# Kernel optimization log

Measured on AMD Instinct MI355X. Metric: run time of the kernel, lower is better.

Reference implementation:

```python
import jax, jax.numpy as jnp
import numpy as np

N_NODES = 100000
N_EDGES = 500000
D = 128        # node feat dim == output dim
DT = 128       # time encoding dim
DE = 128       # edge feat dim
B = 300
K = 2
NN = 20
N_HEADS = 2
N_LAYERS = 2


def setup_inputs() -> dict:
    key = jax.random.key(0)
    ks = jax.random.split(key, 20)
    s = 0.05
    inp = {
        "node_features": jax.random.normal(ks[0], (N_NODES, D), jnp.float32) * s,
        "edge_features": jax.random.normal(ks[1], (N_EDGES, DE), jnp.float32) * s,
        "time_w": jax.random.normal(ks[2], (1, DT), jnp.float32),
        "time_b": jax.random.normal(ks[3], (DT,), jnp.float32),
        "Wq": jax.random.normal(ks[4], (N_LAYERS, D + DT, D), jnp.float32) * s,
        "Wk": jax.random.normal(ks[5], (N_LAYERS, D + DT + DE, D), jnp.float32) * s,
        "Wv": jax.random.normal(ks[6], (N_LAYERS, D + DT + DE, D), jnp.float32) * s,
        "Wo": jax.random.normal(ks[7], (N_LAYERS, D, D), jnp.float32) * s,
        "fc1": jax.random.normal(ks[8], (N_LAYERS, 2 * D, D), jnp.float32) * s,
        "fc2": jax.random.normal(ks[9], (N_LAYERS, D, D), jnp.float32) * s,
        "source_nodes": jax.random.randint(ks[10], (B,), 0, N_NODES),
        "timestamps": jax.random.uniform(ks[11], (B,), jnp.float32, 500.0, 1000.0),
        "neigh2": jax.random.randint(ks[12], (B, K, NN), 0, N_NODES),
        "eidx2": jax.random.randint(ks[13], (B, K, NN), 0, N_EDGES),
        "etimes2": jax.random.uniform(ks[14], (B, K, NN), jnp.float32, 0.0, 500.0),
        "neigh1": jax.random.randint(ks[15], (B * K * NN, K, NN), 0, N_NODES),
        "eidx1": jax.random.randint(ks[16], (B * K * NN, K, NN), 0, N_EDGES),
        "etimes1": jax.random.uniform(ks[17], (B * K * NN, K, NN), jnp.float32, 0.0, 500.0),
    }
    return inp


def reference(node_features, edge_features, time_w, time_b,
              Wq, Wk, Wv, Wo, fc1, fc2,
              source_nodes, timestamps,
              neigh2, eidx2, etimes2,
              neigh1, eidx1, etimes1):
    d = node_features.shape[1]
    dh = d // N_HEADS

    def time_enc(t):  # t: [...] -> [..., DT], TGAT-style cosine time encoding
        return jnp.cos(t[..., None] * time_w[0] + time_b)

    def hop_agg(layer, src_nodes, ts, neigh, eidx, etimes, neigh_emb):
        # neigh/eidx/etimes: [b, K, NN]; neigh_emb: [b, K, NN, d]
        b = src_nodes.shape[0]
        kn = K * NN
        src = node_features[src_nodes]                         # [b, d]
        src_t = time_enc(jnp.zeros((b,), ts.dtype))            # [b, DT]
        deltas = ts[:, None, None] - etimes                    # [b, K, NN]
        et = time_enc(deltas.reshape(b, kn))                   # [b, kn, DT]
        ef = edge_features[eidx].reshape(b, kn, -1)            # [b, kn, DE]
        ne = neigh_emb.reshape(b, kn, -1)                      # [b, kn, d]
        mask = neigh.reshape(b, kn) == 0                       # padded neighbors

        q = jnp.concatenate([src, src_t], axis=-1) @ Wq[layer]            # [b, d]
        kv_in = jnp.concatenate([ne, et, ef], axis=-1)                    # [b, kn, d+DT+DE]
        kk = kv_in @ Wk[layer]                                            # [b, kn, d]
        vv = kv_in @ Wv[layer]

        qh = q.reshape(b, N_HEADS, dh)
        kh = kk.reshape(b, kn, N_HEADS, dh)
        vh = vv.reshape(b, kn, N_HEADS, dh)
        scores = jnp.einsum('bhd,bnhd->bhn', qh, kh) / jnp.sqrt(jnp.float32(dh))
        scores = jnp.where(mask[:, None, :], jnp.float32(-1e9), scores)
        attn = jax.nn.softmax(scores, axis=-1)                            # [b, h, kn]
        out = jnp.einsum('bhn,bnhd->bhd', attn, vh).reshape(b, d) @ Wo[layer]
        merged = jnp.concatenate([out, src], axis=-1)                     # [b, 2d]
        return jax.nn.relu(merged @ fc1[layer]) @ fc2[layer]              # [b, d]

    # --- recursion unrolled (n_layers = 2) ---
    # level 0: raw node features of 2-hop neighbors
    b1 = neigh2.shape[0] * K * NN
    emb0 = node_features[neigh1.reshape(-1)].reshape(b1, K, NN, d)
    ts1 = jnp.repeat(timestamps, K * NN)
    # level 1 aggregation (attention_models[0])
    emb1 = hop_agg(0, neigh2.reshape(-1), ts1, neigh1, eidx1, etimes1, emb0)
    # level 2 aggregation (attention_models[1])
    emb2 = hop_agg(1, source_nodes, timestamps,
                   neigh2, eidx2, etimes2,
                   emb1.reshape(source_nodes.shape[0], K, NN, d))
    return emb2
```

## Files before the change

### kernel.cpp

```cpp
#include <hip/hip_runtime.h>
#include <cstdint>

typedef _Float16 half_t;
typedef _Float16 half8  __attribute__((ext_vector_type(8)));
typedef _Float16 half4_t __attribute__((ext_vector_type(4)));
typedef _Float16 h2f    __attribute__((ext_vector_type(2)));
typedef float    floatx4 __attribute__((ext_vector_type(4)));

#define KNN 40
#define KVPAD 124

#define WS_NF16    0ull
#define WS_EMB16   25600000ull
#define WS_WKVT    28672000ull
#define WS_WQ4     29065216ull
#define WS_W1A4    29196288ull
#define WS_W1B4    29327360ull
#define WS_W24     29458432ull
#define WS_QBIAS   29589504ull
#define WS_WOFTMP  29590528ull
#define WS_ZERO    29721600ull
#define WS_EF16    29721856ull
#define WS_TOTAL_FULL (WS_EF16 + 128000000ull)

__device__ __forceinline__ void ld16(const void* g, void* l) {
  __builtin_amdgcn_global_load_lds(
      (const __attribute__((address_space(1))) unsigned int*)(uintptr_t)g,
      (__attribute__((address_space(3))) unsigned int*)(uintptr_t)l, 16, 0, 0);
}

__device__ __forceinline__ float dot4(half4_t a, half4_t b, float s) {
  s = __builtin_amdgcn_fdot2((h2f){a[0], a[1]}, (h2f){b[0], b[1]}, s, false);
  s = __builtin_amdgcn_fdot2((h2f){a[2], a[3]}, (h2f){b[2], b[3]}, s, false);
  return s;
}

__global__ __launch_bounds__(256) void cvt_kernel(
    const float* __restrict__ src, half_t* __restrict__ dst, int n8) {
  int stride = gridDim.x * 256;
  for (int i = blockIdx.x * 256 + threadIdx.x; i < n8; i += stride) {
    float4 a = *((const float4*)src + 2 * (size_t)i);
    float4 b = *((const float4*)src + 2 * (size_t)i + 1);
    half8 h;
    h[0] = (half_t)a.x; h[1] = (half_t)a.y; h[2] = (half_t)a.z; h[3] = (half_t)a.w;
    h[4] = (half_t)b.x; h[5] = (half_t)b.y; h[6] = (half_t)b.z; h[7] = (half_t)b.w;
    *((half8*)dst + i) = h;
  }
}

#define PK_DECODE(t) int l = (t) >> 14; int u = (t) & 16383; \
  int d4 = u >> 9; int v = u & 511; int j = v >> 2; int e = v & 3;

__global__ __launch_bounds__(256) void precompute_w(
    const float* __restrict__ Wq, const float* __restrict__ Wk,
    const float* __restrict__ Wv, const float* __restrict__ Wo,
    const float* __restrict__ fc1, const float* __restrict__ fc2,
    const float* __restrict__ time_b,
    half_t* __restrict__ WkvT, float* __restrict__ qbias,
    float* __restrict__ woftmp, half_t* __restrict__ Wq4,
    half_t* __restrict__ W1b4, half_t* __restrict__ W24,
    half_t* __restrict__ zrow)
{
  int blk = blockIdx.x, tid = threadIdx.x;
  if (blk < 768) {
    int t = blk * 256 + tid;
    int l = t / 98304;
    int r = t - l * 98304;
    int n = r / 384;
    int k = r - n * 384;
    float vv = (n < 128) ? Wk[l * 49152 + k * 128 + n]
                         : Wv[l * 49152 + k * 128 + (n - 128)];
    WkvT[t] = (half_t)vv;
  } else if (blk == 768) {
    if (tid < 128) zrow[tid] = (half_t)0.f;
    int l = tid >> 7, j = tid & 127;
    float s = 0.f;
    for (int d = 0; d < 128; ++d)
      s += cosf(time_b[d]) * Wq[l * 32768 + (128 + d) * 128 + j];
    qbias[l * 128 + j] = s;
  } else if (blk < 897) {
    int t = (blk - 769) * 256 + tid;
    int l = t >> 14;
    int r = t & 16383;
    int dd = r >> 7, j = r & 127;
    float s = 0.f;
    for (int m = 0; m < 128; ++m)
      s += Wo[l * 16384 + dd * 128 + m] * fc1[l * 32768 + m * 128 + j];
    woftmp[t] = s;
  } else if (blk < 1025) {
    int t = (blk - 897) * 256 + tid;
    PK_DECODE(t);
    Wq4[t] = (half_t)Wq[l * 32768 + (4 * d4 + e) * 128 + j];
  } else if (blk < 1153) {
    int t = (blk - 1025) * 256 + tid;
    PK_DECODE(t);
    W1b4[t] = (half_t)fc1[l * 32768 + (128 + 4 * d4 + e) * 128 + j];
  } else {
    int t = (blk - 1153) * 256 + tid;
    PK_DECODE(t);
    W24[t] = (half_t)fc2[l * 16384 + (4 * d4 + e) * 128 + j];
  }
}

__global__ __launch_bounds__(256) void precompute_w2(
    const float* __restrict__ woftmp, half_t* __restrict__ W1a4) {
  int t = blockIdx.x * 256 + threadIdx.x;
  PK_DECODE(t);
  W1a4[t] = (half_t)woftmp[l * 16384 + (4 * d4 + e) * 128 + j];
}

template <bool EF16, bool L1DIR>
__global__ __launch_bounds__(512, 4) void hop_kernel(
    const float*  __restrict__ nf,
    const half_t* __restrict__ ne16,
    const half_t* __restrict__ ef16,
    const float*  __restrict__ ef32,
    const int*    __restrict__ src_idx,
    const float*  __restrict__ tsv,
    const int*    __restrict__ neigh,
    const int*    __restrict__ eidx,
    const float*  __restrict__ etimes,
    const float*  __restrict__ tw,
    const float*  __restrict__ tb,
    const half_t* __restrict__ Wq4_l,
    const float*  __restrict__ qbias_l,
    const half_t* __restrict__ WkvT_l,
    const half_t* __restrict__ W1a4_l,
    const half_t* __restrict__ W1b4_l,
    const half_t* __restrict__ W24_l,
    const half_t* __restrict__ zrow,
    half_t* __restrict__ out16,
    float*  __restrict__ out32)
{
  __shared__ __align__(16) char smem[71360];
  half_t* BTs  = (half_t*)(smem + 32768);
  half_t* kvT  = (half_t*)(smem + 32768);
  float*  tw_s = (float*)(smem + 65536);
  float*  tb_s = (float*)(smem + 66048);
  float*  qs   = (float*)(smem + 66560);
  half_t* s16  = (half_t*)(smem + 68096);
  half_t* aO16 = (half_t*)(smem + 68864);
  half_t* h116 = (half_t*)(smem + 69632);
  float*  scs  = (float*)(smem + 70400);

  const int tid = threadIdx.x;
  const int bbase = blockIdx.x * 3;
  const int lane = tid & 63, wv = tid >> 6;
  const int l15 = lane & 15, q4 = lane >> 4;
  const int wm = (wv & 1) * 64, wn = (wv >> 1) * 64;

  if (tid < 128) { tw_s[tid] = tw[tid]; tb_s[tid] = tb[tid]; }
  if (tid < 96) {
    int g = tid >> 5, d4 = tid & 31;
    float4 v4 = *(const float4*)(nf + (size_t)src_idx[bbase + g] * 128 + d4 * 4);
    half4_t h;
    h[0] = (half_t)v4.x; h[1] = (half_t)v4.y; h[2] = (half_t)v4.z; h[3] = (half_t)v4.w;
    *(half4_t*)(s16 + g * 128 + d4 * 4) = h;
  }

  int neighval = 1;
  if (tid < 240) {
    int g = tid / 80, rem = tid - g * 80, n = rem % 40;
    neighval = neigh[(bbase + g) * KNN + n];
  }

  const int r = wv * 16 + l15;
  const bool valid = (r < 120);
  float dval = 0.f;
  const half_t* pNE = zrow + q4 * 8;
  const half_t* pEF = zrow + q4 * 8;
  if (valid) {
    int g = r / 40, n = r - g * 40;
    int bg = bbase + g;
    int rowidx = bg * KNN + n;
    dval = tsv[L1DIR ? bg : (bg / 40)] - etimes[rowidx];
    pNE = (L1DIR ? ne16 + (size_t)rowidx * 128
                 : ne16 + (size_t)neigh[rowidx] * 128) + q4 * 8;
    if (EF16) pEF = ef16 + (size_t)eidx[rowidx] * 128 + q4 * 8;
  }
  const float* gbe32 = nullptr;
  const int rr = tid >> 2, pp = tid & 3;
  if (!EF16 && rr < 120) {
    int g2 = rr / 40, n2 = rr - g2 * 40;
    gbe32 = ef32 + (size_t)eidx[(bbase + g2) * KNN + n2] * 128 + pp * 8;
  }

  const half_t* bBase = WkvT_l + (size_t)(2 * wv * 16 + l15) * 384 + q4 * 8;

  floatx4 acc[4][4];
  #pragma unroll
  for (int mi = 0; mi < 4; ++mi)
    #pragma unroll
    for (int ni = 0; ni < 4; ++ni) acc[mi][ni] = (floatx4){0.f, 0.f, 0.f, 0.f};

  auto issB = [&](int s, char* bb) {
    int kc = (s < 4) ? s : (s < 8 ? s + 4 : s - 4);
    const half_t* bp = bBase + kc * 32;
    ld16(bp,        bb + wv * 2048);
    ld16(bp + 6144, bb + wv * 2048 + 1024);
  };
  auto issA = [&](int s, char* ab) {
    const half_t* p = (s < 4) ? pNE + s * 32 : pEF + (s - 4) * 32;
    ld16(p, ab + wv * 1024);
  };
  auto cosA = [&](int s, char* ab) {
    int cb = (s - 8) * 32 + q4 * 8;
    half8 h;
    #pragma unroll
    for (int j = 0; j < 8; ++j) {
      float ang = __builtin_fmaf(dval, tw_s[cb + j], tb_s[cb + j]);
      h[j] = valid ? (half_t)__cosf(ang) : (half_t)0.f;
    }
    *(half8*)(ab + wv * 1024 + lane * 16) = h;
  };
  auto efA32 = [&](int s, char* ab) {
    half8 h = {};
    if (rr < 120) {
      const float* gb = gbe32 + (s - 4) * 32;
      float4 v0 = ((const float4*)gb)[0];
      float4 v1 = ((const float4*)gb)[1];
      h[0] = (half_t)v0.x; h[1] = (half_t)v0.y; h[2] = (half_t)v0.z; h[3] = (half_t)v0.w;
      h[4] = (half_t)v1.x; h[5] = (half_t)v1.y; h[6] = (half_t)v1.z; h[7] = (half_t)v1.w;
    }
    *(half8*)(ab + (rr >> 4) * 1024 + pp * 256 + (rr & 15) * 16) = h;
  };
  auto mfma_step = [&](const char* ab, const char* bb) {
    const half_t* A  = (const half_t*)ab;
    const half_t* Bp = (const half_t*)bb;
    half8 a[4];
    #pragma unroll
    for (int mi = 0; mi < 4; ++mi)
      a[mi] = *(const half8*)(A + ((wv & 1) * 4 + mi) * 512 + q4 * 128 + l15 * 8);
    #pragma unroll
    for (int ni = 0; ni < 4; ++ni) {
      half8 bfr = *(const half8*)(Bp + (((wn >> 4) + ni) * 512) + q4 * 128 + l15 * 8);
      #pragma unroll
      for (int mi = 0; mi < 4; ++mi)
        acc[mi][ni] = __builtin_amdgcn_mfma_f32_16x16x32_f16(a[mi], bfr, acc[mi][ni], 0, 0, 0);
    }
  };
  auto stageW = [&](const half_t* wsrc, char* dst) {
    const char* sw = (const char*)wsrc + wv * 4096 + lane * 16;
    char* dw = dst + wv * 4096;
    ld16(sw, dw); ld16(sw + 1024, dw + 1024);
    ld16(sw + 2048, dw + 2048); ld16(sw + 3072, dw + 3072);
  };

#define AB(i) (smem + (i) * 8192)
#define BB(i) (smem + 32768 + (i) * 16384)
#define FENCE asm volatile("" ::: "memory")

  FENCE;
  issB(0, BB(0)); issB(1, BB(1));
  issA(0, AB(0)); issA(1, AB(1)); issA(2, AB(2)); issA(3, AB(3));
  asm volatile("s_waitcnt lgkmcnt(0)" ::: "memory");
  __builtin_amdgcn_s_barrier(); FENCE;

#define HSTEP(s, WE, WF, ...)                                                   \
  asm volatile("s_waitcnt vmcnt(%0) lgkmcnt(0)" :: "i"(EF16 ? (WE) : (WF))      \
               : "memory");                                                     \
  __builtin_amdgcn_s_barrier(); FENCE;                                          \
  mfma_step(AB((s) & 3), BB((s) & 1));                                          \
  FENCE; __builtin_amdgcn_s_barrier(); FENCE;                                   \
  __VA_ARGS__

  HSTEP(0, 3, 3, issB(2, BB(0)); if constexpr (EF16) issA(4, AB(0)); else efA32(4, AB(0));)
  HSTEP(1, 5, 4, issB(3, BB(1)); if constexpr (EF16) issA(5, AB(1)); else efA32(5, AB(1));)
  HSTEP(2, 7, 5, issB(4, BB(0)); if constexpr (EF16) issA(6, AB(2)); else efA32(6, AB(2));)
  HSTEP(3, 9, 6, issB(5, BB(1)); if constexpr (EF16) issA(7, AB(3)); else efA32(7, AB(3));)
  HSTEP(4, 4, 2, issB(6, BB(0)); cosA(8, AB(0));)
  HSTEP(5, 3, 2, issB(7, BB(1)); cosA(9, AB(1));)
  HSTEP(6, 2, 2, issB(8, BB(0)); cosA(10, AB(2));)
  HSTEP(7, 2, 2, issB(9, BB(1)); cosA(11, AB(3));)
  HSTEP(8, 2, 2, issB(10, BB(0));)
  HSTEP(9, 2, 2, issB(11, BB(1));)
  HSTEP(10, 2, 2, )
  HSTEP(11, 0, 0, )
#undef HSTEP

  stageW(W1a4_l, smem);

  if (wv < 4) {
    #pragma unroll
    for (int mi = 0; mi < 4; ++mi) {
      int row0 = wm + mi * 16 + q4 * 4;
      if (row0 < 120) {
        #pragma unroll
        for (int ni = 0; ni < 4; ++ni) {
          int col = wn + ni * 16 + l15;
          half4_t h;
          h[0] = (half_t)acc[mi][ni][0]; h[1] = (half_t)acc[mi][ni][1];
          h[2] = (half_t)acc[mi][ni][2]; h[3] = (half_t)acc[mi][ni][3];
          *(half4_t*)(kvT + col * KVPAD + row0) = h;
        }
      }
    }
  }

  if (tid < 384) {
    int gq = tid >> 7, jj = tid & 127;
    float s = qbias_l[jj];
    #pragma unroll 8
    for (int d4 = 0; d4 < 32; ++d4) {
      half4_t w = *(const half4_t*)(Wq4_l + (d4 * 128 + jj) * 4);
      half4_t a = *(const half4_t*)(s16 + gq * 128 + d4 * 4);
      s = dot4(w, a, s);
    }
    qs[gq * 128 + jj] = s;
  }
  asm volatile("s_waitcnt lgkmcnt(0)" ::: "memory");
  __builtin_amdgcn_s_barrier(); FENCE;

  if (tid < 240) {
    int g = tid / 80;
    int rem = tid - g * 80;
    int hh = rem / 40;
    int n = rem - hh * 40;
    const float* qrow = qs + g * 128 + hh * 64;
    int row = g * 40 + n;
    float s = 0.f;
    #pragma unroll 8
    for (int d = 0; d < 64; ++d)
      s += qrow[d] * (float)kvT[(hh * 64 + d) * KVPAD + row];
    scs[tid] = (neighval == 0) ? -1e9f : s * 0.125f;
  }
  asm volatile("s_waitcnt lgkmcnt(0)" ::: "memory");
  __builtin_amdgcn_s_barrier(); FENCE;

  if (wv < 6) {
    float v = (lane < 40) ? scs[wv * 40 + lane] : -1e30f;
    float m = v;
    #pragma unroll
    for (int o = 32; o; o >>= 1) m = fmaxf(m, __shfl_xor(m, o));
    float e = (lane < 40) ? __expf(v - m) : 0.f;
    float ssum = e;
    #pragma unroll
    for (int o = 32; o; o >>= 1) ssum += __shfl_xor(ssum, o);
    if (lane < 40) scs[wv * 40 + lane] = e / ssum;
  }
  if (wv >= 4) {
    #pragma unroll
    for (int mi = 0; mi < 4; ++mi) {
      int row0 = wm + mi * 16 + q4 * 4;
      if (row0 < 120) {
        #pragma unroll
        for (int ni = 0; ni < 4; ++ni) {
          int col = wn - 128 + ni * 16 + l15;
          half4_t h;
          h[0] = (half_t)acc[mi][ni][0]; h[1] = (half_t)acc[mi][ni][1];
          h[2] = (half_t)acc[mi][ni][2]; h[3] = (half_t)acc[mi][ni][3];
          *(half4_t*)(kvT + col * KVPAD + row0) = h;
        }
      }
    }
  }
  asm volatile("s_waitcnt lgkmcnt(0)" ::: "memory");
  __builtin_amdgcn_s_barrier(); FENCE;

  if (tid < 384) {
    int g = tid >> 7, dcol = tid & 127, hh = dcol >> 6;
    const float* attn = scs + (g * 2 + hh) * 40;
    const half_t* vcol = kvT + dcol * KVPAD + g * 40;
    float s = 0.f;
    #pragma unroll 8
    for (int n = 0; n < 40; ++n) s += attn[n] * (float)vcol[n];
    aO16[g * 128 + dcol] = (half_t)s;
  }
  asm volatile("s_waitcnt lgkmcnt(0)" ::: "memory");
  __builtin_amdgcn_s_barrier(); FENCE;

  stageW(W1b4_l, (char*)BTs);
  asm volatile("s_waitcnt vmcnt(4)" ::: "memory");
  __builtin_amdgcn_s_barrier(); FENCE;

  float p1 = 0.f;
  if (tid < 384) {
    int g = tid >> 7, jj = tid & 127;
    #pragma unroll 8
    for (int d4 = 0; d4 < 32; ++d4) {
      half4_t w = *(const half4_t*)((const half_t*)smem + (d4 * 128 + jj) * 4);
      half4_t a = *(const half4_t*)(aO16 + g * 128 + d4 * 4);
      p1 = dot4(w, a, p1);
    }
  }
  FENCE; __builtin_amdgcn_s_barrier(); FENCE;

  stageW(W24_l, smem);
  asm volatile("s_waitcnt vmcnt(4)" ::: "memory");
  __builtin_amdgcn_s_barrier(); FENCE;
  if (tid < 384) {
    int g = tid >> 7, jj = tid & 127;
    float p2 = p1;
    #pragma unroll 8
    for (int d4 = 0; d4 < 32; ++d4) {
      half4_t w = *(const half4_t*)(BTs + (d4 * 128 + jj) * 4);
      half4_t a = *(const half4_t*)(s16 + g * 128 + d4 * 4);
      p2 = dot4(w, a, p2);
    }
    h116[g * 128 + jj] = (half_t)fmaxf(p2, 0.f);
  }
  asm volatile("s_waitcnt vmcnt(0) lgkmcnt(0)" ::: "memory");
  __builtin_amdgcn_s_barrier(); FENCE;

  if (tid < 384) {
    int g = tid >> 7, ii = tid & 127;
    float s = 0.f;
    #pragma unroll 8
    for (int j4 = 0; j4 < 32; ++j4) {
      half4_t w = *(const half4_t*)((const half_t*)smem + (j4 * 128 + ii) * 4);
      half4_t a = *(const half4_t*)(h116 + g * 128 + j4 * 4);
      s = dot4(w, a, s);
    }
    if (L1DIR) out32[(size_t)(bbase + g) * 128 + ii] = s;
    else       out16[(size_t)(bbase + g) * 128 + ii] = (half_t)s;
  }
#undef AB
#undef BB
#undef FENCE
}

extern "C" void kernel_launch(void* const* d_in, const int* in_sizes, int n_in,
                              void* d_out, int out_size, void* d_ws, size_t ws_size,
                              hipStream_t stream) {
  const float* nf      = (const float*)d_in[0];
  const float* ef      = (const float*)d_in[1];
  const float* tw      = (const float*)d_in[2];
  const float* tb      = (const float*)d_in[3];
  const float* Wq      = (const float*)d_in[4];
  const float* Wk      = (const float*)d_in[5];
  const float* Wv      = (const float*)d_in[6];
  const float* Wo      = (const float*)d_in[7];
  const float* fc1     = (const float*)d_in[8];
  const float* fc2     = (const float*)d_in[9];
  const int*   srcn    = (const int*)d_in[10];
  const float* ts      = (const float*)d_in[11];
  const int*   neigh2  = (const int*)d_in[12];
  const int*   eidx2   = (const int*)d_in[13];
  const float* etimes2 = (const float*)d_in[14];
  const int*   neigh1  = (const int*)d_in[15];
  const int*   eidx1   = (const int*)d_in[16];
  const float* etimes1 = (const float*)d_in[17];

  char* ws = (char*)d_ws;
  half_t* nf16   = (half_t*)(ws + WS_NF16);
  half_t* emb116 = (half_t*)(ws + WS_EMB16);
  half_t* WkvT16 = (half_t*)(ws + WS_WKVT);
  half_t* Wq4    = (half_t*)(ws + WS_WQ4);
  half_t* W1a4   = (half_t*)(ws + WS_W1A4);
  half_t* W1b4   = (half_t*)(ws + WS_W1B4);
  half_t* W24    = (half_t*)(ws + WS_W24);
  float*  qbias  = (float*)(ws + WS_QBIAS);
  float*  woftmp = (float*)(ws + WS_WOFTMP);
  half_t* zrow   = (half_t*)(ws + WS_ZERO);
  half_t* ef16   = (half_t*)(ws + WS_EF16);

  bool full = (ws_size >= WS_TOTAL_FULL);

  cvt_kernel<<<dim3(2048), dim3(256), 0, stream>>>(nf, nf16, 1600000);
  if (full)
    cvt_kernel<<<dim3(4096), dim3(256), 0, stream>>>(ef, ef16, 8000000);
  precompute_w<<<dim3(1281), dim3(256), 0, stream>>>(
      Wq, Wk, Wv, Wo, fc1, fc2, tb, WkvT16, qbias, woftmp, Wq4, W1b4, W24, zrow);
  precompute_w2<<<dim3(128), dim3(256), 0, stream>>>(woftmp, W1a4);

  if (full) {
    hop_kernel<true, false><<<dim3(4000), dim3(512), 0, stream>>>(
        nf, nf16, ef16, ef, neigh2, ts, neigh1, eidx1, etimes1, tw, tb,
        Wq4, qbias, WkvT16, W1a4, W1b4, W24, zrow, emb116, nullptr);
    hop_kernel<true, true><<<dim3(100), dim3(512), 0, stream>>>(
        nf, emb116, ef16, ef, srcn, ts, neigh2, eidx2, etimes2, tw, tb,
        Wq4 + 16384, qbias + 128, WkvT16 + 98304, W1a4 + 16384, W1b4 + 16384,
        W24 + 16384, zrow, emb116, (float*)d_out);
  } else {
    hop_kernel<false, false><<<dim3(4000), dim3(512), 0, stream>>>(
        nf, nf16, ef16, ef, neigh2, ts, neigh1, eidx1, etimes1, tw, tb,
        Wq4, qbias, WkvT16, W1a4, W1b4, W24, zrow, emb116, nullptr);
    hop_kernel<false, true><<<dim3(100), dim3(512), 0, stream>>>(
        nf, emb116, ef16, ef, srcn, ts, neigh2, eidx2, etimes2, tw, tb,
        Wq4 + 16384, qbias + 128, WkvT16 + 98304, W1a4 + 16384, W1b4 + 16384,
        W24 + 16384, zrow, emb116, (float*)d_out);
  }
}
```

Before: 706.4 us.

## Use MFMA for output MLP and read weights directly from global memory

The post-attention fc1/fc2 matvecs, previously done as scalar fdot2 loops over LDS-staged weights, become 16x16x32 MFMA tiles. Only 3 of 16 rows are real, and B fragments are loaded straight from global memory. The LDS weight staging and its barriers are removed. Packed weight layouts widen from 4 to 8 halves so the Q projection can use half8 loads, and the score and AV loops are vectorised with float4 and half4 loads. This trades redundant MFMA rows and uncoalesced global weight reads for fewer barriers and fewer scalar dot instructions.

```diff
diff --git a/kernel.cpp b/kernel.cpp
--- a/kernel.cpp
+++ b/kernel.cpp
@@ -29,9 +29,11 @@
       (__attribute__((address_space(3))) unsigned int*)(uintptr_t)l, 16, 0, 0);
 }
 
-__device__ __forceinline__ float dot4(half4_t a, half4_t b, float s) {
+__device__ __forceinline__ float dot8(half8 a, half8 b, float s) {
   s = __builtin_amdgcn_fdot2((h2f){a[0], a[1]}, (h2f){b[0], b[1]}, s, false);
   s = __builtin_amdgcn_fdot2((h2f){a[2], a[3]}, (h2f){b[2], b[3]}, s, false);
+  s = __builtin_amdgcn_fdot2((h2f){a[4], a[5]}, (h2f){b[4], b[5]}, s, false);
+  s = __builtin_amdgcn_fdot2((h2f){a[6], a[7]}, (h2f){b[6], b[7]}, s, false);
   return s;
 }
 
@@ -48,8 +50,8 @@
   }
 }
 
-#define PK_DECODE(t) int l = (t) >> 14; int u = (t) & 16383; \
-  int d4 = u >> 9; int v = u & 511; int j = v >> 2; int e = v & 3;
+#define PK8_DECODE(t) int l = (t) >> 14; int u = (t) & 16383; \
+  int d8 = u >> 10; int v = u & 1023; int j = v >> 3; int e = v & 7;
 
 __global__ __launch_bounds__(256) void precompute_w(
     const float* __restrict__ Wq, const float* __restrict__ Wk,
@@ -89,24 +91,24 @@
     woftmp[t] = s;
   } else if (blk < 1025) {
     int t = (blk - 897) * 256 + tid;
-    PK_DECODE(t);
-    Wq4[t] = (half_t)Wq[l * 32768 + (4 * d4 + e) * 128 + j];
+    PK8_DECODE(t);
+    Wq4[t] = (half_t)Wq[l * 32768 + (8 * d8 + e) * 128 + j];
   } else if (blk < 1153) {
     int t = (blk - 1025) * 256 + tid;
-    PK_DECODE(t);
-    W1b4[t] = (half_t)fc1[l * 32768 + (128 + 4 * d4 + e) * 128 + j];
+    PK8_DECODE(t);
+    W1b4[t] = (half_t)fc1[l * 32768 + (128 + 8 * d8 + e) * 128 + j];
   } else {
     int t = (blk - 1153) * 256 + tid;
-    PK_DECODE(t);
-    W24[t] = (half_t)fc2[l * 16384 + (4 * d4 + e) * 128 + j];
+    PK8_DECODE(t);
+    W24[t] = (half_t)fc2[l * 16384 + (8 * d8 + e) * 128 + j];
   }
 }
 
 __global__ __launch_bounds__(256) void precompute_w2(
     const float* __restrict__ woftmp, half_t* __restrict__ W1a4) {
   int t = blockIdx.x * 256 + threadIdx.x;
-  PK_DECODE(t);
-  W1a4[t] = (half_t)woftmp[l * 16384 + (4 * d4 + e) * 128 + j];
+  PK8_DECODE(t);
+  W1a4[t] = (half_t)woftmp[l * 16384 + (8 * d8 + e) * 128 + j];
 }
 
 template <bool EF16, bool L1DIR>
@@ -239,12 +241,6 @@
         acc[mi][ni] = __builtin_amdgcn_mfma_f32_16x16x32_f16(a[mi], bfr, acc[mi][ni], 0, 0, 0);
     }
   };
-  auto stageW = [&](const half_t* wsrc, char* dst) {
-    const char* sw = (const char*)wsrc + wv * 4096 + lane * 16;
-    char* dw = dst + wv * 4096;
-    ld16(sw, dw); ld16(sw + 1024, dw + 1024);
-    ld16(sw + 2048, dw + 2048); ld16(sw + 3072, dw + 3072);
-  };
 
 #define AB(i) (smem + (i) * 8192)
 #define BB(i) (smem + 32768 + (i) * 16384)
@@ -278,7 +274,6 @@
   HSTEP(11, 0, 0, )
 #undef HSTEP
 
-  stageW(W1a4_l, smem);
 
   if (wv < 4) {
     #pragma unroll
@@ -300,11 +295,11 @@
   if (tid < 384) {
     int gq = tid >> 7, jj = tid & 127;
     float s = qbias_l[jj];
-    #pragma unroll 8
-    for (int d4 = 0; d4 < 32; ++d4) {
-      half4_t w = *(const half4_t*)(Wq4_l + (d4 * 128 + jj) * 4);
-      half4_t a = *(const half4_t*)(s16 + gq * 128 + d4 * 4);
-      s = dot4(w, a, s);
+    #pragma unroll
+    for (int d8 = 0; d8 < 16; ++d8) {
+      half8 w = *(const half8*)(Wq4_l + (d8 * 128 + jj) * 8);
+      half8 a = *(const half8*)(s16 + gq * 128 + d8 * 8);
+      s = dot8(w, a, s);
     }
     qs[gq * 128 + jj] = s;
   }
@@ -316,12 +311,18 @@
     int rem = tid - g * 80;
     int hh = rem / 40;
     int n = rem - hh * 40;
-    const float* qrow = qs + g * 128 + hh * 64;
+    const float4* qrow4 = (const float4*)(qs + g * 128 + hh * 64);
     int row = g * 40 + n;
     float s = 0.f;
-    #pragma unroll 8
-    for (int d = 0; d < 64; ++d)
-      s += qrow[d] * (float)kvT[(hh * 64 + d) * KVPAD + row];
+    #pragma unroll
+    for (int d4 = 0; d4 < 16; ++d4) {
+      float4 qv = qrow4[d4];
+      const half_t* kp = kvT + (hh * 64 + d4 * 4) * KVPAD + row;
+      s += qv.x * (float)kp[0];
+      s += qv.y * (float)kp[KVPAD];
+      s += qv.z * (float)kp[2 * KVPAD];
+      s += qv.w * (float)kp[3 * KVPAD];
+    }
     scs[tid] = (neighval == 0) ? -1e9f : s * 0.125f;
   }
   asm volatile("s_waitcnt lgkmcnt(0)" ::: "memory");
@@ -359,60 +360,81 @@
 
   if (tid < 384) {
     int g = tid >> 7, dcol = tid & 127, hh = dcol >> 6;
-    const float* attn = scs + (g * 2 + hh) * 40;
+    const float4* at4 = (const float4*)(scs + (g * 2 + hh) * 40);
     const half_t* vcol = kvT + dcol * KVPAD + g * 40;
     float s = 0.f;
-    #pragma unroll 8
-    for (int n = 0; n < 40; ++n) s += attn[n] * (float)vcol[n];
+    #pragma unroll
+    for (int n4 = 0; n4 < 10; ++n4) {
+      float4 a4 = at4[n4];
+      half4_t v = *(const half4_t*)(vcol + n4 * 4);
+      s += a4.x * (float)v[0] + a4.y * (float)v[1]
+         + a4.z * (float)v[2] + a4.w * (float)v[3];
+    }
     aO16[g * 128 + dcol] = (half_t)s;
   }
   asm volatile("s_waitcnt lgkmcnt(0)" ::: "memory");
   __builtin_amdgcn_s_barrier(); FENCE;
 
-  stageW(W1b4_l, (char*)BTs);
-  asm volatile("s_waitcnt vmcnt(4)" ::: "memory");
+  {
+    const int ar = (l15 < 3) ? l15 : 0;
+    if (wv < 4) {
+      const int ni0 = wv * 2;
+      floatx4 facc0 = (floatx4){0.f, 0.f, 0.f, 0.f};
+      floatx4 facc1 = (floatx4){0.f, 0.f, 0.f, 0.f};
+      #pragma unroll
+      for (int kc = 0; kc < 4; ++kc) {
+        half8 a1 = *(const half8*)(aO16 + ar * 128 + kc * 32 + q4 * 8);
+        half8 a2 = *(const half8*)(s16  + ar * 128 + kc * 32 + q4 * 8);
+        int kb = (kc * 4 + q4) * 128;
+        half8 b1a = *(const half8*)(W1a4_l + (size_t)(kb + ni0 * 16 + l15) * 8);
+        half8 b1b = *(const half8*)(W1a4_l + (size_t)(kb + ni0 * 16 + 16 + l15) * 8);
+        half8 b2a = *(const half8*)(W1b4_l + (size_t)(kb + ni0 * 16 + l15) * 8);
+        half8 b2b = *(const half8*)(W1b4_l + (size_t)(kb + ni0 * 16 + 16 + l15) * 8);
+        facc0 = __builtin_amdgcn_mfma_f32_16x16x32_f16(a1, b1a, facc0, 0, 0, 0);
+        facc1 = __builtin_amdgcn_mfma_f32_16x16x32_f16(a1, b1b, facc1, 0, 0, 0);
+        facc0 = __builtin_amdgcn_mfma_f32_16x16x32_f16(a2, b2a, facc0, 0, 0, 0);
+        facc1 = __builtin_amdgcn_mfma_f32_16x16x32_f16(a2, b2b, facc1, 0, 0, 0);
+      }
+      if (q4 == 0) {
+        #pragma unroll
+        for (int e = 0; e < 3; ++e) {
+          h116[e * 128 + ni0 * 16 + l15]       = (half_t)fmaxf(facc0[e], 0.f);
+          h116[e * 128 + (ni0 + 1) * 16 + l15] = (half_t)fmaxf(facc1[e], 0.f);
+        }
+      }
+    }
+  }
+  asm volatile("s_waitcnt lgkmcnt(0)" ::: "memory");
   __builtin_amdgcn_s_barrier(); FENCE;
 
-  float p1 = 0.f;
-  if (tid < 384) {
-    int g = tid >> 7, jj = tid & 127;
-    #pragma unroll 8
-    for (int d4 = 0; d4 < 32; ++d4) {
-      half4_t w = *(const half4_t*)((const half_t*)smem + (d4 * 128 + jj) * 4);
-      half4_t a = *(const half4_t*)(aO16 + g * 128 + d4 * 4);
-      p1 = dot4(w, a, p1);
-    }
-  }
-  FENCE; __builtin_amdgcn_s_barrier(); FENCE;
-
-  stageW(W24_l, smem);
-  asm volatile("s_waitcnt vmcnt(4)" ::: "memory");
-  __builtin_amdgcn_s_barrier(); FENCE;
-  if (tid < 384) {
-    int g = tid >> 7, jj = tid & 127;
-    float p2 = p1;
-    #pragma unroll 8
-    for (int d4 = 0; d4 < 32; ++d4) {
-      half4_t w = *(const half4_t*)(BTs + (d4 * 128 + jj) * 4);
-      half4_t a = *(const half4_t*)(s16 + g * 128 + d4 * 4);
-      p2 = dot4(w, a, p2);
-    }
-    h116[g * 128 + jj] = (half_t)fmaxf(p2, 0.f);
-  }
-  asm volatile("s_waitcnt vmcnt(0) lgkmcnt(0)" ::: "memory");
-  __builtin_amdgcn_s_barrier(); FENCE;
-
-  if (tid < 384) {
-    int g = tid >> 7, ii = tid & 127;
-    float s = 0.f;
-    #pragma unroll 8
-    for (int j4 = 0; j4 < 32; ++j4) {
-      half4_t w = *(const half4_t*)((const half_t*)smem + (j4 * 128 + ii) * 4);
-      half4_t a = *(const half4_t*)(h116 + g * 128 + j4 * 4);
-      s = dot4(w, a, s);
-    }
-    if (L1DIR) out32[(size_t)(bbase + g) * 128 + ii] = s;
-    else       out16[(size_t)(bbase + g) * 128 + ii] = (half_t)s;
+  {
+    const int ar = (l15 < 3) ? l15 : 0;
+    if (wv < 4) {
+      const int ni0 = wv * 2;
+      floatx4 facc0 = (floatx4){0.f, 0.f, 0.f, 0.f};
+      floatx4 facc1 = (floatx4){0.f, 0.f, 0.f, 0.f};
+      #pragma unroll
+      for (int kc = 0; kc < 4; ++kc) {
+        half8 a = *(const half8*)(h116 + ar * 128 + kc * 32 + q4 * 8);
+        int kb = (kc * 4 + q4) * 128;
+        half8 ba = *(const half8*)(W24_l + (size_t)(kb + ni0 * 16 + l15) * 8);
+        half8 bb = *(const half8*)(W24_l + (size_t)(kb + ni0 * 16 + 16 + l15) * 8);
+        facc0 = __builtin_amdgcn_mfma_f32_16x16x32_f16(a, ba, facc0, 0, 0, 0);
+        facc1 = __builtin_amdgcn_mfma_f32_16x16x32_f16(a, bb, facc1, 0, 0, 0);
+      }
+      if (q4 == 0) {
+        #pragma unroll
+        for (int e = 0; e < 3; ++e) {
+          if (L1DIR) {
+            out32[(size_t)(bbase + e) * 128 + ni0 * 16 + l15]       = facc0[e];
+            out32[(size_t)(bbase + e) * 128 + (ni0 + 1) * 16 + l15] = facc1[e];
+          } else {
+            out16[(size_t)(bbase + e) * 128 + ni0 * 16 + l15]       = (half_t)facc0[e];
+            out16[(size_t)(bbase + e) * 128 + (ni0 + 1) * 16 + l15] = (half_t)facc1[e];
+          }
+        }
+      }
+    }
   }
 #undef AB
 #undef BB
```

Result: faster. 688.2 us (-2.6%).
